# Kernel optimization log

Hardware: AMD Instinct MI355X
Metric: run time of the kernel (lower is better)

The kernel has to match this reference:

```python
import jax, jax.numpy as jnp
import numpy as np

B, S, E = 16, 1024, 1024  # flattened-softmax view requires S == E
EPS = 1e-5


def _ln(x, g, b):
    mu = jnp.mean(x, axis=-1, keepdims=True)
    var = jnp.var(x, axis=-1, keepdims=True)
    return (x - mu) * jax.lax.rsqrt(var + EPS) * g + b


def setup_inputs() -> dict:
    key = jax.random.key(0)
    ks = jax.random.split(key, 7)
    sc = 1.0 / np.sqrt(E)
    return {
        "pl_source": jax.random.normal(ks[0], (B, S, E), jnp.float32),
        "sam_source": jax.random.normal(ks[1], (B, S, E), jnp.float32),
        "Wq": jax.random.normal(ks[2], (E, E), jnp.float32) * sc,
        "Wk": jax.random.normal(ks[3], (E, E), jnp.float32) * sc,
        "Wv": jax.random.normal(ks[4], (E, E), jnp.float32) * sc,
        "ln1_g": jnp.ones((E,), jnp.float32),
        "ln1_b": jnp.zeros((E,), jnp.float32),
        "W1": jax.random.normal(ks[5], (E, 2 * E), jnp.float32) * sc,
        "W2": jax.random.normal(ks[6], (2 * E, E), jnp.float32) * (1.0 / np.sqrt(2 * E)),
        "ln2_g": jnp.ones((E,), jnp.float32),
        "ln2_b": jnp.zeros((E,), jnp.float32),
    }


def reference(pl_source, sam_source, Wq, Wk, Wv, ln1_g, ln1_b, W1, W2, ln2_g, ln2_b):
    q = jnp.einsum('bse,ef->bsf', pl_source, Wq)
    k = jnp.einsum('bse,ef->bsf', sam_source, Wk)
    v = jnp.einsum('bse,ef->bsf', sam_source, Wv)
    # scores [B,S,S], scaled by sqrt(head dim of q)
    scores = jnp.einsum('bsf,btf->bst', q, k) / jnp.sqrt(jnp.asarray(E, q.dtype))
    # non-standard: softmax over the WHOLE flattened score matrix per batch
    w = jax.nn.softmax(scores.reshape(B, S * S), axis=-1).reshape(B, S, E)  # S == E
    attn = jnp.einsum('bst,bte->bse', w, v)
    x = _ln(attn + pl_source, ln1_g, ln1_b)
    ff = jnp.einsum('bsh,he->bse', jnp.einsum('bse,eh->bsh', x, W1), W2)
    return _ln(ff + x, ln2_g, ln2_b)
```

## Files before the change

kernel.cpp:

```cpp
#include <hip/hip_runtime.h>
#include <hip/hip_bf16.h>
#include <type_traits>


typedef float  f32x4  __attribute__((ext_vector_type(4)));
typedef unsigned short u16x8 __attribute__((ext_vector_type(8)));
typedef unsigned short u16x4 __attribute__((ext_vector_type(4)));
typedef __bf16 bf16x8 __attribute__((ext_vector_type(8)));

__device__ __forceinline__ unsigned short f2bf(float f) {
  unsigned int u = __float_as_uint(f);
  u += 0x7fffu + ((u >> 16) & 1u);
  return (unsigned short)(u >> 16);
}
__device__ __forceinline__ float bf2f(unsigned short h) {
  return __uint_as_float(((unsigned int)h) << 16);
}

template<int SPLIT>
__device__ __forceinline__ void cvt8(const float4& a, const float4& b, u16x8& h, u16x8& l) {
  float f[8] = {a.x, a.y, a.z, a.w, b.x, b.y, b.z, b.w};
#pragma unroll
  for (int i = 0; i < 8; ++i) {
    unsigned short hb = f2bf(f[i]);
    h[i] = hb;
    if constexpr (SPLIT) l[i] = f2bf(f[i] - bf2f(hb));
  }
}

template<int AM, int BM, int CM>
__global__ __launch_bounds__(256, 2)
void gemm(const void* __restrict__ Av, const void* __restrict__ Bv,
          void* __restrict__ Cv, int M, int N, int K, int lda, int ldb,
          long sA, long sB, long sC, float scale, float beta)
{
  constexpr bool SA = (AM == 2), SB = (BM == 2);
  constexpr int NB = 2 + (SA ? 1 : 0) + (SB ? 1 : 0);
  constexpr int IAL = 2;
  constexpr int IBL = SA ? 3 : 2;
  __shared__ unsigned short sh[NB][4][128][8];

  const int t    = threadIdx.x;
  const int lane = t & 63;
  const int wave = t >> 6;
  const int wm   = (wave >> 1) << 6;
  const int wn   = (wave & 1) << 6;
  const int bm   = blockIdx.x << 7;
  const int bn   = blockIdx.y << 7;
  const int r_   = t >> 1;
  const int g_   = t & 1;

  const unsigned short* A16 = (const unsigned short*)Av + (size_t)blockIdx.z * sA + (size_t)(bm + r_) * lda + (g_ << 3);
  const float*          A32 = (const float*)Av          + (size_t)blockIdx.z * sA + (size_t)(bm + r_) * lda + (g_ << 3);
  const unsigned short* B16 = (const unsigned short*)Bv + (size_t)blockIdx.z * sB + (size_t)(bn + r_) * ldb + (g_ << 3);
  const float*          B32 = (const float*)Bv          + (size_t)blockIdx.z * sB + (size_t)(bn + r_) * ldb + (g_ << 3);

  f32x4 acc[4][4];
#pragma unroll
  for (int mi = 0; mi < 4; ++mi)
#pragma unroll
    for (int ni = 0; ni < 4; ++ni)
      acc[mi][ni] = (f32x4){0.f, 0.f, 0.f, 0.f};

  u16x8 ha0, ha1, hb0, hb1;
  float4 fa0, fa1, fa2, fa3, fb0, fb1, fb2, fb3;

  auto loadAB = [&](int kt) {
    const int ko = kt << 5;
    if constexpr (AM == 0) {
      ha0 = *(const u16x8*)(A16 + ko);
      ha1 = *(const u16x8*)(A16 + ko + 16);
    } else {
      fa0 = *(const float4*)(A32 + ko);      fa1 = *(const float4*)(A32 + ko + 4);
      fa2 = *(const float4*)(A32 + ko + 16); fa3 = *(const float4*)(A32 + ko + 20);
    }
    if constexpr (BM == 0) {
      hb0 = *(const u16x8*)(B16 + ko);
      hb1 = *(const u16x8*)(B16 + ko + 16);
    } else {
      fb0 = *(const float4*)(B32 + ko);      fb1 = *(const float4*)(B32 + ko + 4);
      fb2 = *(const float4*)(B32 + ko + 16); fb3 = *(const float4*)(B32 + ko + 20);
    }
  };
  loadAB(0);

  const int NT = K >> 5;
  const int kg = lane >> 4;
  const int lr = lane & 15;

  for (int kt = 0; kt < NT; ++kt) {
    __syncthreads();
    if constexpr (AM == 0) {
      *(u16x8*)&sh[0][g_][r_][0]     = ha0;
      *(u16x8*)&sh[0][g_ + 2][r_][0] = ha1;
    } else {
      u16x8 h, l;
      cvt8<SA>(fa0, fa1, h, l);
      *(u16x8*)&sh[0][g_][r_][0] = h;     if constexpr (SA) *(u16x8*)&sh[IAL][g_][r_][0] = l;
      cvt8<SA>(fa2, fa3, h, l);
      *(u16x8*)&sh[0][g_ + 2][r_][0] = h; if constexpr (SA) *(u16x8*)&sh[IAL][g_ + 2][r_][0] = l;
    }
    if constexpr (BM == 0) {
      *(u16x8*)&sh[1][g_][r_][0]     = hb0;
      *(u16x8*)&sh[1][g_ + 2][r_][0] = hb1;
    } else {
      u16x8 h, l;
      cvt8<SB>(fb0, fb1, h, l);
      *(u16x8*)&sh[1][g_][r_][0] = h;     if constexpr (SB) *(u16x8*)&sh[IBL][g_][r_][0] = l;
      cvt8<SB>(fb2, fb3, h, l);
      *(u16x8*)&sh[1][g_ + 2][r_][0] = h; if constexpr (SB) *(u16x8*)&sh[IBL][g_ + 2][r_][0] = l;
    }
    __syncthreads();

    if (kt + 1 < NT) loadAB(kt + 1);

    u16x8 va_[4], vb_[4], val_[4], vbl_[4];
#pragma unroll
    for (int mi = 0; mi < 4; ++mi) {
      va_[mi] = *(const u16x8*)&sh[0][kg][wm + (mi << 4) + lr][0];
      if constexpr (SA) val_[mi] = *(const u16x8*)&sh[IAL][kg][wm + (mi << 4) + lr][0];
    }
#pragma unroll
    for (int ni = 0; ni < 4; ++ni) {
      vb_[ni] = *(const u16x8*)&sh[1][kg][wn + (ni << 4) + lr][0];
      if constexpr (SB) vbl_[ni] = *(const u16x8*)&sh[IBL][kg][wn + (ni << 4) + lr][0];
    }
#pragma unroll
    for (int mi = 0; mi < 4; ++mi)
#pragma unroll
      for (int ni = 0; ni < 4; ++ni) {
        acc[mi][ni] = __builtin_amdgcn_mfma_f32_16x16x32_bf16(
            __builtin_bit_cast(bf16x8, va_[mi]), __builtin_bit_cast(bf16x8, vb_[ni]),
            acc[mi][ni], 0, 0, 0);
        if constexpr (SB)
          acc[mi][ni] = __builtin_amdgcn_mfma_f32_16x16x32_bf16(
              __builtin_bit_cast(bf16x8, va_[mi]), __builtin_bit_cast(bf16x8, vbl_[ni]),
              acc[mi][ni], 0, 0, 0);
        if constexpr (SA)
          acc[mi][ni] = __builtin_amdgcn_mfma_f32_16x16x32_bf16(
              __builtin_bit_cast(bf16x8, val_[mi]), __builtin_bit_cast(bf16x8, vb_[ni]),
              acc[mi][ni], 0, 0, 0);
      }
  }

  const size_t cbase = (size_t)blockIdx.z * sC;
#pragma unroll
  for (int mi = 0; mi < 4; ++mi)
#pragma unroll
    for (int ni = 0; ni < 4; ++ni) {
      const int row0 = bm + wm + (mi << 4) + ((lane >> 4) << 2);
      const int col  = bn + wn + (ni << 4) + lr;
#pragma unroll
      for (int i = 0; i < 4; ++i) {
        float val = acc[mi][ni][i] * scale;
        const size_t idx = cbase + (size_t)(row0 + i) * N + col;
        if constexpr (CM == 0) {
          float* C = (float*)Cv;
          if (beta != 0.f) val += beta * C[idx];
          C[idx] = val;
        } else {
          ((unsigned short*)Cv)[idx] = f2bf(val);
        }
      }
    }
}

template<typename IT, typename OT>
__global__ __launch_bounds__(256)
void transpose_k(const IT* __restrict__ in, OT* __restrict__ out,
                 int R, int C, long sIn, long sOut)
{
  __shared__ float tile[32][33];
  in  += (size_t)blockIdx.z * sIn;
  out += (size_t)blockIdx.z * sOut;
  const int tx = threadIdx.x, ty = threadIdx.y;
  const int c0 = blockIdx.x << 5, r0 = blockIdx.y << 5;
#pragma unroll
  for (int i = 0; i < 4; ++i) {
    int r = ty + (i << 3);
    float v;
    if constexpr (std::is_same_v<IT, unsigned short>)
      v = bf2f(in[(size_t)(r0 + r) * C + c0 + tx]);
    else
      v = in[(size_t)(r0 + r) * C + c0 + tx];
    tile[r][tx] = v;
  }
  __syncthreads();
#pragma unroll
  for (int i = 0; i < 4; ++i) {
    int r = ty + (i << 3);
    float v = tile[tx][r];
    if constexpr (std::is_same_v<OT, unsigned short>)
      out[(size_t)(c0 + r) * R + r0 + tx] = f2bf(v);
    else
      out[(size_t)(c0 + r) * R + r0 + tx] = v;
  }
}

__global__ __launch_bounds__(256)
void softmax_pass1(const float* __restrict__ sc, float2* __restrict__ part)
{
  const int b = blockIdx.y;
  const float* p = sc + ((size_t)b << 20) + ((size_t)blockIdx.x << 12);
  const int t = threadIdx.x;
  float v[16];
#pragma unroll
  for (int i = 0; i < 4; ++i) {
    float4 f = *(const float4*)(p + (t << 2) + (i << 10));
    v[i * 4 + 0] = f.x; v[i * 4 + 1] = f.y; v[i * 4 + 2] = f.z; v[i * 4 + 3] = f.w;
  }
  float m = v[0];
#pragma unroll
  for (int i = 1; i < 16; ++i) m = fmaxf(m, v[i]);
  for (int off = 32; off; off >>= 1) m = fmaxf(m, __shfl_down(m, off));
  __shared__ float red[8];
  if ((t & 63) == 0) red[t >> 6] = m;
  __syncthreads();
  m = fmaxf(fmaxf(red[0], red[1]), fmaxf(red[2], red[3]));
  float s = 0.f;
#pragma unroll
  for (int i = 0; i < 16; ++i) s += __expf(v[i] - m);
  for (int off = 32; off; off >>= 1) s += __shfl_down(s, off);
  if ((t & 63) == 0) red[4 + (t >> 6)] = s;
  __syncthreads();
  if (t == 0) part[(b << 8) + blockIdx.x] = make_float2(m, red[4] + red[5] + red[6] + red[7]);
}

__global__ __launch_bounds__(256)
void softmax_pass2(const float2* __restrict__ part, float2* __restrict__ bstats)
{
  const int b = blockIdx.x, t = threadIdx.x;
  float2 pr = part[(b << 8) + t];
  float m = pr.x;
  for (int off = 32; off; off >>= 1) m = fmaxf(m, __shfl_down(m, off));
  __shared__ float red[8];
  if ((t & 63) == 0) red[t >> 6] = m;
  __syncthreads();
  m = fmaxf(fmaxf(red[0], red[1]), fmaxf(red[2], red[3]));
  float s = pr.y * __expf(pr.x - m);
  for (int off = 32; off; off >>= 1) s += __shfl_down(s, off);
  __shared__ float red2[4];
  if ((t & 63) == 0) red2[t >> 6] = s;
  __syncthreads();
  if (t == 0) bstats[b] = make_float2(m, 1.f / (red2[0] + red2[1] + red2[2] + red2[3]));
}

__global__ __launch_bounds__(256)
void softmax_pass3(const float* __restrict__ sc, unsigned short* __restrict__ wb,
                   const float2* __restrict__ bst)
{
  const int b = blockIdx.y;
  const float2 st = bst[b];
  const size_t off = ((size_t)b << 20) + ((size_t)blockIdx.x << 12) + ((size_t)threadIdx.x << 2);
  const float* p = sc + off;
  unsigned short* o = wb + off;
#pragma unroll
  for (int i = 0; i < 4; ++i) {
    float4 f = *(const float4*)(p + (i << 10));
    u16x4 u;
    u[0] = f2bf(__expf(f.x - st.x) * st.y);
    u[1] = f2bf(__expf(f.y - st.x) * st.y);
    u[2] = f2bf(__expf(f.z - st.x) * st.y);
    u[3] = f2bf(__expf(f.w - st.x) * st.y);
    *(u16x4*)(o + (i << 10)) = u;
  }
}

template<typename TA>
__global__ __launch_bounds__(256)
void ln_fused(const TA* __restrict__ a, const float* __restrict__ res,
              const float* __restrict__ g, const float* __restrict__ bb,
              float* __restrict__ out)
{
  const size_t base = (size_t)blockIdx.x << 10;
  const int t = threadIdx.x;
  float x0, x1, x2, x3;
  if constexpr (std::is_same_v<TA, unsigned short>) {
    u16x4 va = *(const u16x4*)(a + base + (t << 2));
    x0 = bf2f(va[0]); x1 = bf2f(va[1]); x2 = bf2f(va[2]); x3 = bf2f(va[3]);
  } else {
    float4 va = *(const float4*)(a + base + (t << 2));
    x0 = va.x; x1 = va.y; x2 = va.z; x3 = va.w;
  }
  float4 vr = *(const float4*)(res + base + (t << 2));
  x0 += vr.x; x1 += vr.y; x2 += vr.z; x3 += vr.w;
  float s = x0 + x1 + x2 + x3;
  float q = x0 * x0 + x1 * x1 + x2 * x2 + x3 * x3;
  for (int off = 32; off; off >>= 1) { s += __shfl_down(s, off); q += __shfl_down(q, off); }
  __shared__ float red[8];
  if ((t & 63) == 0) { red[t >> 6] = s; red[4 + (t >> 6)] = q; }
  __syncthreads();
  float S = red[0] + red[1] + red[2] + red[3];
  float Q = red[4] + red[5] + red[6] + red[7];
  float mu   = S * 0.0009765625f;
  float rstd = rsqrtf(Q * 0.0009765625f - mu * mu + 1e-5f);
  float4 vg = *(const float4*)(g + (t << 2));
  float4 vb = *(const float4*)(bb + (t << 2));
  float4 o;
  o.x = (x0 - mu) * rstd * vg.x + vb.x;
  o.y = (x1 - mu) * rstd * vg.y + vb.y;
  o.z = (x2 - mu) * rstd * vg.z + vb.z;
  o.w = (x3 - mu) * rstd * vg.w + vb.w;
  *(float4*)(out + base + (t << 2)) = o;
}

extern "C" void kernel_launch(void* const* d_in, const int* in_sizes, int n_in,
                              void* d_out, int out_size, void* d_ws, size_t ws_size,
                              hipStream_t stream)
{
  const float* pl  = (const float*)d_in[0];
  const float* sam = (const float*)d_in[1];
  const float* Wq  = (const float*)d_in[2];
  const float* Wk  = (const float*)d_in[3];
  const float* Wv  = (const float*)d_in[4];
  const float* g1  = (const float*)d_in[5];
  const float* b1  = (const float*)d_in[6];
  const float* W1  = (const float*)d_in[7];
  const float* W2  = (const float*)d_in[8];
  const float* g2  = (const float*)d_in[9];
  const float* b2  = (const float*)d_in[10];

  char* wsb = (char*)d_ws;
  const size_t MB = 1ull << 20;
  unsigned short* WqTb = (unsigned short*)(wsb + 0 * MB);
  unsigned short* WkTb = (unsigned short*)(wsb + 2 * MB);
  unsigned short* WvTb = (unsigned short*)(wsb + 4 * MB);
  float*  W1T  = (float*)(wsb + 6 * MB);
  float*  W2T  = (float*)(wsb + 14 * MB);
  unsigned short* qb   = (unsigned short*)(wsb + 22 * MB);
  unsigned short* kb   = (unsigned short*)(wsb + 54 * MB);
  unsigned short* vb   = (unsigned short*)(wsb + 86 * MB);
  unsigned short* vTb  = (unsigned short*)(wsb + 118 * MB);
  float*  hbuf  = (float*)(wsb + 86 * MB);
  float*  ffbuf = (float*)(wsb + 22 * MB);
  float*  sc    = (float*)(wsb + 150 * MB);
  float*  xbuf  = sc;
  float2* part  = (float2*)(wsb + 214 * MB);
  float2* bst   = (float2*)(wsb + 214 * MB + 65536);
  unsigned short* attnb = qb;
  unsigned short* wb_   = kb;

  const long M1 = 1 << 20;
  dim3 tb(32, 8);

  transpose_k<float, unsigned short><<<dim3(32, 32, 1), tb, 0, stream>>>(Wq, WqTb, 1024, 1024, 0, 0);
  transpose_k<float, unsigned short><<<dim3(32, 32, 1), tb, 0, stream>>>(Wk, WkTb, 1024, 1024, 0, 0);
  transpose_k<float, unsigned short><<<dim3(32, 32, 1), tb, 0, stream>>>(Wv, WvTb, 1024, 1024, 0, 0);
  transpose_k<float, float><<<dim3(64, 32, 1), tb, 0, stream>>>(W1, W1T, 1024, 2048, 0, 0);
  transpose_k<float, float><<<dim3(32, 64, 1), tb, 0, stream>>>(W2, W2T, 2048, 1024, 0, 0);

  gemm<1, 0, 1><<<dim3(128, 8, 1), 256, 0, stream>>>(pl,  WqTb, qb, 16384, 1024, 1024, 1024, 1024, 0, 0, 0, 1.f, 0.f);
  gemm<1, 0, 1><<<dim3(128, 8, 1), 256, 0, stream>>>(sam, WkTb, kb, 16384, 1024, 1024, 1024, 1024, 0, 0, 0, 1.f, 0.f);
  gemm<1, 0, 1><<<dim3(128, 8, 1), 256, 0, stream>>>(sam, WvTb, vb, 16384, 1024, 1024, 1024, 1024, 0, 0, 0, 1.f, 0.f);

  transpose_k<unsigned short, unsigned short><<<dim3(32, 32, 16), tb, 0, stream>>>(vb, vTb, 1024, 1024, M1, M1);

  gemm<0, 0, 0><<<dim3(8, 8, 16), 256, 0, stream>>>(qb, kb, sc, 1024, 1024, 1024, 1024, 1024, M1, M1, M1, 0.03125f, 0.f);

  softmax_pass1<<<dim3(256, 16, 1), 256, 0, stream>>>(sc, part);
  softmax_pass2<<<16, 256, 0, stream>>>(part, bst);
  softmax_pass3<<<dim3(256, 16, 1), 256, 0, stream>>>(sc, wb_, bst);

  gemm<0, 0, 1><<<dim3(8, 8, 16), 256, 0, stream>>>(wb_, vTb, attnb, 1024, 1024, 1024, 1024, 1024, M1, M1, M1, 1.f, 0.f);

  ln_fused<unsigned short><<<16384, 256, 0, stream>>>(attnb, pl, g1, b1, xbuf);

  gemm<2, 2, 0><<<dim3(128, 8, 1), 256, 0, stream>>>(xbuf, W1T,              hbuf,  16384, 1024, 1024, 1024, 1024, 0, 0, 0, 1.f, 0.f);
  gemm<2, 2, 0><<<dim3(128, 8, 1), 256, 0, stream>>>(hbuf, W2T,              ffbuf, 16384, 1024, 1024, 1024, 2048, 0, 0, 0, 1.f, 0.f);
  gemm<2, 2, 0><<<dim3(128, 8, 1), 256, 0, stream>>>(xbuf, W1T + (1024*1024), hbuf,  16384, 1024, 1024, 1024, 1024, 0, 0, 0, 1.f, 0.f);
  gemm<2, 2, 0><<<dim3(128, 8, 1), 256, 0, stream>>>(hbuf, W2T + 1024,        ffbuf, 16384, 1024, 1024, 1024, 2048, 0, 0, 0, 1.f, 1.f);

  ln_fused<float><<<16384, 256, 0, stream>>>(ffbuf, xbuf, g2, b2, (float*)d_out);
}
```

Baseline: 1.137 ms.

## Rework GEMM pipeline around 16-bit inputs with fp16 hi/lo split for FFN

```diff
diff --git a/kernel.cpp b/kernel.cpp
--- a/kernel.cpp
+++ b/kernel.cpp
@@ -1,44 +1,39 @@
 #include <hip/hip_runtime.h>
-#include <hip/hip_bf16.h>
-#include <type_traits>
-
-
-typedef float  f32x4  __attribute__((ext_vector_type(4)));
+
+
+typedef float  f32x4 __attribute__((ext_vector_type(4)));
+typedef unsigned short u16;
 typedef unsigned short u16x8 __attribute__((ext_vector_type(8)));
 typedef unsigned short u16x4 __attribute__((ext_vector_type(4)));
 typedef __bf16 bf16x8 __attribute__((ext_vector_type(8)));
-
-__device__ __forceinline__ unsigned short f2bf(float f) {
+typedef _Float16 f16x8 __attribute__((ext_vector_type(8)));
+
+__device__ __forceinline__ u16 f2bf(float f) {
   unsigned int u = __float_as_uint(f);
   u += 0x7fffu + ((u >> 16) & 1u);
-  return (unsigned short)(u >> 16);
-}
-__device__ __forceinline__ float bf2f(unsigned short h) {
+  return (u16)(u >> 16);
+}
+__device__ __forceinline__ float bf2f(u16 h) {
   return __uint_as_float(((unsigned int)h) << 16);
 }
-
-template<int SPLIT>
-__device__ __forceinline__ void cvt8(const float4& a, const float4& b, u16x8& h, u16x8& l) {
-  float f[8] = {a.x, a.y, a.z, a.w, b.x, b.y, b.z, b.w};
-#pragma unroll
-  for (int i = 0; i < 8; ++i) {
-    unsigned short hb = f2bf(f[i]);
-    h[i] = hb;
-    if constexpr (SPLIT) l[i] = f2bf(f[i] - bf2f(hb));
-  }
-}
-
-template<int AM, int BM, int CM>
-__global__ __launch_bounds__(256, 2)
-void gemm(const void* __restrict__ Av, const void* __restrict__ Bv,
-          void* __restrict__ Cv, int M, int N, int K, int lda, int ldb,
-          long sA, long sB, long sC, float scale, float beta)
-{
-  constexpr bool SA = (AM == 2), SB = (BM == 2);
-  constexpr int NB = 2 + (SA ? 1 : 0) + (SB ? 1 : 0);
-  constexpr int IAL = 2;
-  constexpr int IBL = SA ? 3 : 2;
-  __shared__ unsigned short sh[NB][4][128][8];
+__device__ __forceinline__ u16 f2h(float f) {
+  _Float16 h = (_Float16)f;
+  return __builtin_bit_cast(unsigned short, h);
+}
+__device__ __forceinline__ float h2f(u16 b) {
+  return (float)__builtin_bit_cast(_Float16, b);
+}
+
+template<int DT, int CM>
+__global__ __launch_bounds__(256)
+void gemm16(const u16* __restrict__ A0, const u16* __restrict__ A1,
+            const u16* __restrict__ B0, const u16* __restrict__ B1,
+            void* __restrict__ C0, void* __restrict__ C1,
+            int M, int N, int nseg, int lda, int ldb,
+            long batchA, long batchB, long batchC, float scale, float beta)
+{
+  __shared__ u16 lA[4096];
+  __shared__ u16 lB[4096];
 
   const int t    = threadIdx.x;
   const int lane = t & 63;
@@ -47,13 +42,20 @@
   const int wn   = (wave & 1) << 6;
   const int bm   = blockIdx.x << 7;
   const int bn   = blockIdx.y << 7;
-  const int r_   = t >> 1;
-  const int g_   = t & 1;
-
-  const unsigned short* A16 = (const unsigned short*)Av + (size_t)blockIdx.z * sA + (size_t)(bm + r_) * lda + (g_ << 3);
-  const float*          A32 = (const float*)Av          + (size_t)blockIdx.z * sA + (size_t)(bm + r_) * lda + (g_ << 3);
-  const unsigned short* B16 = (const unsigned short*)Bv + (size_t)blockIdx.z * sB + (size_t)(bn + r_) * ldb + (g_ << 3);
-  const float*          B32 = (const float*)Bv          + (size_t)blockIdx.z * sB + (size_t)(bn + r_) * ldb + (g_ << 3);
+
+  A0 += (size_t)blockIdx.z * batchA;  A1 += (size_t)blockIdx.z * batchA;
+  B0 += (size_t)blockIdx.z * batchB;  B1 += (size_t)blockIdx.z * batchB;
+
+  const int sr  = t >> 2;
+  const int scc = (t & 3) << 3;
+  const size_t aoff0 = (size_t)(bm + sr) * lda + scc;
+  const size_t aoff1 = (size_t)(bm + 64 + sr) * lda + scc;
+  const size_t boff0 = (size_t)(bn + sr) * ldb + scc;
+  const size_t boff1 = (size_t)(bn + 64 + sr) * ldb + scc;
+  u16* sA0 = &lA[t << 3];
+  u16* sA1 = &lA[2048 + (t << 3)];
+  u16* sB0 = &lB[t << 3];
+  u16* sB1 = &lB[2048 + (t << 3)];
 
   f32x4 acc[4][4];
 #pragma unroll
@@ -62,88 +64,56 @@
     for (int ni = 0; ni < 4; ++ni)
       acc[mi][ni] = (f32x4){0.f, 0.f, 0.f, 0.f};
 
-  u16x8 ha0, ha1, hb0, hb1;
-  float4 fa0, fa1, fa2, fa3, fb0, fb1, fb2, fb3;
-
-  auto loadAB = [&](int kt) {
-    const int ko = kt << 5;
-    if constexpr (AM == 0) {
-      ha0 = *(const u16x8*)(A16 + ko);
-      ha1 = *(const u16x8*)(A16 + ko + 16);
-    } else {
-      fa0 = *(const float4*)(A32 + ko);      fa1 = *(const float4*)(A32 + ko + 4);
-      fa2 = *(const float4*)(A32 + ko + 16); fa3 = *(const float4*)(A32 + ko + 20);
-    }
-    if constexpr (BM == 0) {
-      hb0 = *(const u16x8*)(B16 + ko);
-      hb1 = *(const u16x8*)(B16 + ko + 16);
-    } else {
-      fb0 = *(const float4*)(B32 + ko);      fb1 = *(const float4*)(B32 + ko + 4);
-      fb2 = *(const float4*)(B32 + ko + 16); fb3 = *(const float4*)(B32 + ko + 20);
-    }
-  };
-  loadAB(0);
-
-  const int NT = K >> 5;
   const int kg = lane >> 4;
   const int lr = lane & 15;
+  const int NT = nseg << 5;
+
+  u16x8 ra0 = *(const u16x8*)(A0 + aoff0);
+  u16x8 ra1 = *(const u16x8*)(A0 + aoff1);
+  u16x8 rb0 = *(const u16x8*)(B0 + boff0);
+  u16x8 rb1 = *(const u16x8*)(B0 + boff1);
 
   for (int kt = 0; kt < NT; ++kt) {
     __syncthreads();
-    if constexpr (AM == 0) {
-      *(u16x8*)&sh[0][g_][r_][0]     = ha0;
-      *(u16x8*)&sh[0][g_ + 2][r_][0] = ha1;
-    } else {
-      u16x8 h, l;
-      cvt8<SA>(fa0, fa1, h, l);
-      *(u16x8*)&sh[0][g_][r_][0] = h;     if constexpr (SA) *(u16x8*)&sh[IAL][g_][r_][0] = l;
-      cvt8<SA>(fa2, fa3, h, l);
-      *(u16x8*)&sh[0][g_ + 2][r_][0] = h; if constexpr (SA) *(u16x8*)&sh[IAL][g_ + 2][r_][0] = l;
+    *(u16x8*)sA0 = ra0;
+    *(u16x8*)sA1 = ra1;
+    *(u16x8*)sB0 = rb0;
+    *(u16x8*)sB1 = rb1;
+    __syncthreads();
+
+    if (kt + 1 < NT) {
+      const u16* As = ((kt + 1) & 32) ? A1 : A0;
+      const u16* Bs = ((kt + 1) & 32) ? B1 : B0;
+      const int ko = ((kt + 1) & 31) << 5;
+      ra0 = *(const u16x8*)(As + aoff0 + ko);
+      ra1 = *(const u16x8*)(As + aoff1 + ko);
+      rb0 = *(const u16x8*)(Bs + boff0 + ko);
+      rb1 = *(const u16x8*)(Bs + boff1 + ko);
     }
-    if constexpr (BM == 0) {
-      *(u16x8*)&sh[1][g_][r_][0]     = hb0;
-      *(u16x8*)&sh[1][g_ + 2][r_][0] = hb1;
-    } else {
-      u16x8 h, l;
-      cvt8<SB>(fb0, fb1, h, l);
-      *(u16x8*)&sh[1][g_][r_][0] = h;     if constexpr (SB) *(u16x8*)&sh[IBL][g_][r_][0] = l;
-      cvt8<SB>(fb2, fb3, h, l);
-      *(u16x8*)&sh[1][g_ + 2][r_][0] = h; if constexpr (SB) *(u16x8*)&sh[IBL][g_ + 2][r_][0] = l;
-    }
-    __syncthreads();
-
-    if (kt + 1 < NT) loadAB(kt + 1);
-
-    u16x8 va_[4], vb_[4], val_[4], vbl_[4];
-#pragma unroll
-    for (int mi = 0; mi < 4; ++mi) {
-      va_[mi] = *(const u16x8*)&sh[0][kg][wm + (mi << 4) + lr][0];
-      if constexpr (SA) val_[mi] = *(const u16x8*)&sh[IAL][kg][wm + (mi << 4) + lr][0];
-    }
-#pragma unroll
-    for (int ni = 0; ni < 4; ++ni) {
-      vb_[ni] = *(const u16x8*)&sh[1][kg][wn + (ni << 4) + lr][0];
-      if constexpr (SB) vbl_[ni] = *(const u16x8*)&sh[IBL][kg][wn + (ni << 4) + lr][0];
-    }
+
+    u16x8 fa[4], fb[4];
 #pragma unroll
     for (int mi = 0; mi < 4; ++mi)
+      fa[mi] = *(const u16x8*)&lA[((wm + (mi << 4) + lr) << 5) + (kg << 3)];
+#pragma unroll
+    for (int ni = 0; ni < 4; ++ni)
+      fb[ni] = *(const u16x8*)&lB[((wn + (ni << 4) + lr) << 5) + (kg << 3)];
+#pragma unroll
+    for (int mi = 0; mi < 4; ++mi)
 #pragma unroll
       for (int ni = 0; ni < 4; ++ni) {
-        acc[mi][ni] = __builtin_amdgcn_mfma_f32_16x16x32_bf16(
-            __builtin_bit_cast(bf16x8, va_[mi]), __builtin_bit_cast(bf16x8, vb_[ni]),
-            acc[mi][ni], 0, 0, 0);
-        if constexpr (SB)
+        if constexpr (DT == 0)
           acc[mi][ni] = __builtin_amdgcn_mfma_f32_16x16x32_bf16(
-              __builtin_bit_cast(bf16x8, va_[mi]), __builtin_bit_cast(bf16x8, vbl_[ni]),
+              __builtin_bit_cast(bf16x8, fa[mi]), __builtin_bit_cast(bf16x8, fb[ni]),
               acc[mi][ni], 0, 0, 0);
-        if constexpr (SA)
-          acc[mi][ni] = __builtin_amdgcn_mfma_f32_16x16x32_bf16(
-              __builtin_bit_cast(bf16x8, val_[mi]), __builtin_bit_cast(bf16x8, vb_[ni]),
+        else
+          acc[mi][ni] = __builtin_amdgcn_mfma_f32_16x16x32_f16(
+              __builtin_bit_cast(f16x8, fa[mi]), __builtin_bit_cast(f16x8, fb[ni]),
               acc[mi][ni], 0, 0, 0);
       }
   }
 
-  const size_t cbase = (size_t)blockIdx.z * sC;
+  const size_t cb = (size_t)blockIdx.z * batchC;
 #pragma unroll
   for (int mi = 0; mi < 4; ++mi)
 #pragma unroll
@@ -152,37 +122,38 @@
       const int col  = bn + wn + (ni << 4) + lr;
 #pragma unroll
       for (int i = 0; i < 4; ++i) {
-        float val = acc[mi][ni][i] * scale;
-        const size_t idx = cbase + (size_t)(row0 + i) * N + col;
+        float v = acc[mi][ni][i] * scale;
+        const size_t idx = cb + (size_t)(row0 + i) * N + col;
         if constexpr (CM == 0) {
-          float* C = (float*)Cv;
-          if (beta != 0.f) val += beta * C[idx];
-          C[idx] = val;
+          float* C = (float*)C0;
+          if (beta != 0.f) v += beta * C[idx];
+          C[idx] = v;
+        } else if constexpr (CM == 1) {
+          ((u16*)C0)[idx] = f2bf(v);
         } else {
-          ((unsigned short*)Cv)[idx] = f2bf(val);
+          u16 hb = f2h(v);
+          ((u16*)C0)[idx] = hb;
+          ((u16*)C1)[idx] = f2h(v - h2f(hb));
         }
       }
     }
 }
 
-template<typename IT, typename OT>
-__global__ __launch_bounds__(256)
-void transpose_k(const IT* __restrict__ in, OT* __restrict__ out,
-                 int R, int C, long sIn, long sOut)
+template<int IM, int OM>
+__global__ __launch_bounds__(256)
+void transpose_cvt(const void* __restrict__ inv, u16* __restrict__ out,
+                   int R, int C, int ldin, int coff, long sIn, long sOut)
 {
   __shared__ float tile[32][33];
-  in  += (size_t)blockIdx.z * sIn;
-  out += (size_t)blockIdx.z * sOut;
   const int tx = threadIdx.x, ty = threadIdx.y;
   const int c0 = blockIdx.x << 5, r0 = blockIdx.y << 5;
 #pragma unroll
   for (int i = 0; i < 4; ++i) {
     int r = ty + (i << 3);
+    size_t idx = (size_t)blockIdx.z * sIn + (size_t)(r0 + r) * ldin + c0 + tx + coff;
     float v;
-    if constexpr (std::is_same_v<IT, unsigned short>)
-      v = bf2f(in[(size_t)(r0 + r) * C + c0 + tx]);
-    else
-      v = in[(size_t)(r0 + r) * C + c0 + tx];
+    if constexpr (IM == 0) v = ((const float*)inv)[idx];
+    else                   v = bf2f(((const u16*)inv)[idx]);
     tile[r][tx] = v;
   }
   __syncthreads();
@@ -190,10 +161,21 @@
   for (int i = 0; i < 4; ++i) {
     int r = ty + (i << 3);
     float v = tile[tx][r];
-    if constexpr (std::is_same_v<OT, unsigned short>)
-      out[(size_t)(c0 + r) * R + r0 + tx] = f2bf(v);
-    else
-      out[(size_t)(c0 + r) * R + r0 + tx] = v;
+    size_t idx = (size_t)blockIdx.z * sOut + (size_t)(c0 + r) * R + r0 + tx;
+    out[idx] = (OM == 1) ? f2bf(v) : f2h(v);
+  }
+}
+
+__global__ __launch_bounds__(256)
+void cvt_bf16k(const float* __restrict__ in, u16* __restrict__ out, int n4)
+{
+  int i = blockIdx.x * 256 + threadIdx.x;
+  const int stride = gridDim.x * 256;
+  for (; i < n4; i += stride) {
+    float4 f = ((const float4*)in)[i];
+    u16x4 o;
+    o[0] = f2bf(f.x); o[1] = f2bf(f.y); o[2] = f2bf(f.z); o[3] = f2bf(f.w);
+    ((u16x4*)out)[i] = o;
   }
 }
 
@@ -246,14 +228,14 @@
 }
 
 __global__ __launch_bounds__(256)
-void softmax_pass3(const float* __restrict__ sc, unsigned short* __restrict__ wb,
+void softmax_pass3(const float* __restrict__ sc, u16* __restrict__ wb,
                    const float2* __restrict__ bst)
 {
   const int b = blockIdx.y;
   const float2 st = bst[b];
   const size_t off = ((size_t)b << 20) + ((size_t)blockIdx.x << 12) + ((size_t)threadIdx.x << 2);
   const float* p = sc + off;
-  unsigned short* o = wb + off;
+  u16* o = wb + off;
 #pragma unroll
   for (int i = 0; i < 4; ++i) {
     float4 f = *(const float4*)(p + (i << 10));
@@ -266,26 +248,35 @@
   }
 }
 
-template<typename TA>
-__global__ __launch_bounds__(256)
-void ln_fused(const TA* __restrict__ a, const float* __restrict__ res,
-              const float* __restrict__ g, const float* __restrict__ bb,
-              float* __restrict__ out)
+template<int AM, int RM, int OM>
+__global__ __launch_bounds__(256)
+void ln_fused(const void* __restrict__ av, const void* __restrict__ r0v,
+              const void* __restrict__ r1v, const float* __restrict__ g,
+              const float* __restrict__ bb, void* __restrict__ o0v,
+              void* __restrict__ o1v)
 {
   const size_t base = (size_t)blockIdx.x << 10;
   const int t = threadIdx.x;
-  float x0, x1, x2, x3;
-  if constexpr (std::is_same_v<TA, unsigned short>) {
-    u16x4 va = *(const u16x4*)(a + base + (t << 2));
-    x0 = bf2f(va[0]); x1 = bf2f(va[1]); x2 = bf2f(va[2]); x3 = bf2f(va[3]);
+  float x[4];
+  if constexpr (AM == 0) {
+    float4 a = *(const float4*)((const float*)av + base + (t << 2));
+    x[0] = a.x; x[1] = a.y; x[2] = a.z; x[3] = a.w;
   } else {
-    float4 va = *(const float4*)(a + base + (t << 2));
-    x0 = va.x; x1 = va.y; x2 = va.z; x3 = va.w;
-  }
-  float4 vr = *(const float4*)(res + base + (t << 2));
-  x0 += vr.x; x1 += vr.y; x2 += vr.z; x3 += vr.w;
-  float s = x0 + x1 + x2 + x3;
-  float q = x0 * x0 + x1 * x1 + x2 * x2 + x3 * x3;
+    u16x4 a = *(const u16x4*)((const u16*)av + base + (t << 2));
+#pragma unroll
+    for (int i = 0; i < 4; ++i) x[i] = bf2f(a[i]);
+  }
+  if constexpr (RM == 0) {
+    float4 r = *(const float4*)((const float*)r0v + base + (t << 2));
+    x[0] += r.x; x[1] += r.y; x[2] += r.z; x[3] += r.w;
+  } else {
+    u16x4 rh = *(const u16x4*)((const u16*)r0v + base + (t << 2));
+    u16x4 rl = *(const u16x4*)((const u16*)r1v + base + (t << 2));
+#pragma unroll
+    for (int i = 0; i < 4; ++i) x[i] += h2f(rh[i]) + h2f(rl[i]);
+  }
+  float s = x[0] + x[1] + x[2] + x[3];
+  float q = x[0]*x[0] + x[1]*x[1] + x[2]*x[2] + x[3]*x[3];
   for (int off = 32; off; off >>= 1) { s += __shfl_down(s, off); q += __shfl_down(q, off); }
   __shared__ float red[8];
   if ((t & 63) == 0) { red[t >> 6] = s; red[4 + (t >> 6)] = q; }
@@ -296,12 +287,24 @@
   float rstd = rsqrtf(Q * 0.0009765625f - mu * mu + 1e-5f);
   float4 vg = *(const float4*)(g + (t << 2));
   float4 vb = *(const float4*)(bb + (t << 2));
-  float4 o;
-  o.x = (x0 - mu) * rstd * vg.x + vb.x;
-  o.y = (x1 - mu) * rstd * vg.y + vb.y;
-  o.z = (x2 - mu) * rstd * vg.z + vb.z;
-  o.w = (x3 - mu) * rstd * vg.w + vb.w;
-  *(float4*)(out + base + (t << 2)) = o;
+  float y[4];
+  y[0] = (x[0] - mu) * rstd * vg.x + vb.x;
+  y[1] = (x[1] - mu) * rstd * vg.y + vb.y;
+  y[2] = (x[2] - mu) * rstd * vg.z + vb.z;
+  y[3] = (x[3] - mu) * rstd * vg.w + vb.w;
+  if constexpr (OM == 0) {
+    float4 o = {y[0], y[1], y[2], y[3]};
+    *(float4*)((float*)o0v + base + (t << 2)) = o;
+  } else {
+    u16x4 oh, ol;
+#pragma unroll
+    for (int i = 0; i < 4; ++i) {
+      oh[i] = f2h(y[i]);
+      ol[i] = f2h(y[i] - h2f(oh[i]));
+    }
+    *(u16x4*)((u16*)o0v + base + (t << 2)) = oh;
+    *(u16x4*)((u16*)o1v + base + (t << 2)) = ol;
+  }
 }
 
 extern "C" void kernel_launch(void* const* d_in, const int* in_sizes, int n_in,
@@ -322,53 +325,64 @@
 
   char* wsb = (char*)d_ws;
   const size_t MB = 1ull << 20;
-  unsigned short* WqTb = (unsigned short*)(wsb + 0 * MB);
-  unsigned short* WkTb = (unsigned short*)(wsb + 2 * MB);
-  unsigned short* WvTb = (unsigned short*)(wsb + 4 * MB);
-  float*  W1T  = (float*)(wsb + 6 * MB);
-  float*  W2T  = (float*)(wsb + 14 * MB);
-  unsigned short* qb   = (unsigned short*)(wsb + 22 * MB);
-  unsigned short* kb   = (unsigned short*)(wsb + 54 * MB);
-  unsigned short* vb   = (unsigned short*)(wsb + 86 * MB);
-  unsigned short* vTb  = (unsigned short*)(wsb + 118 * MB);
-  float*  hbuf  = (float*)(wsb + 86 * MB);
-  float*  ffbuf = (float*)(wsb + 22 * MB);
-  float*  sc    = (float*)(wsb + 150 * MB);
-  float*  xbuf  = sc;
-  float2* part  = (float2*)(wsb + 214 * MB);
-  float2* bst   = (float2*)(wsb + 214 * MB + 65536);
-  unsigned short* attnb = qb;
-  unsigned short* wb_   = kb;
-
-  const long M1 = 1 << 20;
+  u16*   plb   = (u16*)(wsb + 0 * MB);
+  u16*   samb  = (u16*)(wsb + 32 * MB);
+  u16*   qb    = (u16*)(wsb + 64 * MB);
+  u16*   vTb   = (u16*)(wsb + 96 * MB);
+  u16*   kvb   = (u16*)(wsb + 128 * MB);
+  float* sc    = (float*)(wsb + 0 * MB);
+  u16*   wb    = qb;
+  u16*   attnb = kvb;
+  u16*   xh    = qb;
+  u16*   xl    = vTb;
+  u16*   hhH   = (u16*)(wsb + 0 * MB);
+  u16*   hlH   = (u16*)(wsb + 32 * MB);
+  float* ff    = (float*)(wsb + 128 * MB);
+  u16*   WqTb  = (u16*)(wsb + 192 * MB);
+  u16*   WkvTb = (u16*)(wsb + 194 * MB);
+  u16*   W1Th  = (u16*)(wsb + 198 * MB);
+  u16*   W2Th  = (u16*)(wsb + 202 * MB);
+  float2* part = (float2*)(wsb + 206 * MB);
+  float2* bst  = (float2*)(wsb + 206 * MB + 65536);
+
+  const long M1 = 1 << 20, M2 = 2 << 20;
   dim3 tb(32, 8);
 
-  transpose_k<float, unsigned short><<<dim3(32, 32, 1), tb, 0, stream>>>(Wq, WqTb, 1024, 1024, 0, 0);
-  transpose_k<float, unsigned short><<<dim3(32, 32, 1), tb, 0, stream>>>(Wk, WkTb, 1024, 1024, 0, 0);
-  transpose_k<float, unsigned short><<<dim3(32, 32, 1), tb, 0, stream>>>(Wv, WvTb, 1024, 1024, 0, 0);
-  transpose_k<float, float><<<dim3(64, 32, 1), tb, 0, stream>>>(W1, W1T, 1024, 2048, 0, 0);
-  transpose_k<float, float><<<dim3(32, 64, 1), tb, 0, stream>>>(W2, W2T, 2048, 1024, 0, 0);
-
-  gemm<1, 0, 1><<<dim3(128, 8, 1), 256, 0, stream>>>(pl,  WqTb, qb, 16384, 1024, 1024, 1024, 1024, 0, 0, 0, 1.f, 0.f);
-  gemm<1, 0, 1><<<dim3(128, 8, 1), 256, 0, stream>>>(sam, WkTb, kb, 16384, 1024, 1024, 1024, 1024, 0, 0, 0, 1.f, 0.f);
-  gemm<1, 0, 1><<<dim3(128, 8, 1), 256, 0, stream>>>(sam, WvTb, vb, 16384, 1024, 1024, 1024, 1024, 0, 0, 0, 1.f, 0.f);
-
-  transpose_k<unsigned short, unsigned short><<<dim3(32, 32, 16), tb, 0, stream>>>(vb, vTb, 1024, 1024, M1, M1);
-
-  gemm<0, 0, 0><<<dim3(8, 8, 16), 256, 0, stream>>>(qb, kb, sc, 1024, 1024, 1024, 1024, 1024, M1, M1, M1, 0.03125f, 0.f);
+  cvt_bf16k<<<2048, 256, 0, stream>>>(pl,  plb,  1 << 22);
+  cvt_bf16k<<<2048, 256, 0, stream>>>(sam, samb, 1 << 22);
+  transpose_cvt<0,1><<<dim3(32, 32, 1), tb, 0, stream>>>(Wq, WqTb, 1024, 1024, 1024, 0, 0, 0);
+  transpose_cvt<0,1><<<dim3(32, 32, 1), tb, 0, stream>>>(Wk, WkvTb, 1024, 1024, 1024, 0, 0, 0);
+  transpose_cvt<0,1><<<dim3(32, 32, 1), tb, 0, stream>>>(Wv, WkvTb + M1, 1024, 1024, 1024, 0, 0, 0);
+  transpose_cvt<0,2><<<dim3(64, 32, 1), tb, 0, stream>>>(W1, W1Th, 1024, 2048, 2048, 0, 0, 0);
+  transpose_cvt<0,2><<<dim3(32, 64, 1), tb, 0, stream>>>(W2, W2Th, 2048, 1024, 1024, 0, 0, 0);
+
+  gemm16<0,1><<<dim3(128, 8, 1), 256, 0, stream>>>(plb, plb, WqTb, WqTb, qb, nullptr,
+      16384, 1024, 1, 1024, 1024, 0, 0, 0, 1.f, 0.f);
+  gemm16<0,1><<<dim3(128, 16, 1), 256, 0, stream>>>(samb, samb, WkvTb, WkvTb, kvb, nullptr,
+      16384, 2048, 1, 1024, 1024, 0, 0, 0, 1.f, 0.f);
+
+  transpose_cvt<1,1><<<dim3(32, 32, 16), tb, 0, stream>>>(kvb, vTb, 1024, 1024, 2048, 1024, M2, M1);
+
+  gemm16<0,0><<<dim3(8, 8, 16), 256, 0, stream>>>(qb, qb, kvb, kvb, sc, nullptr,
+      1024, 1024, 1, 1024, 2048, M1, M2, M1, 0.03125f, 0.f);
 
   softmax_pass1<<<dim3(256, 16, 1), 256, 0, stream>>>(sc, part);
   softmax_pass2<<<16, 256, 0, stream>>>(part, bst);
-  softmax_pass3<<<dim3(256, 16, 1), 256, 0, stream>>>(sc, wb_, bst);
-
-  gemm<0, 0, 1><<<dim3(8, 8, 16), 256, 0, stream>>>(wb_, vTb, attnb, 1024, 1024, 1024, 1024, 1024, M1, M1, M1, 1.f, 0.f);
-
-  ln_fused<unsigned short><<<16384, 256, 0, stream>>>(attnb, pl, g1, b1, xbuf);
-
-  gemm<2, 2, 0><<<dim3(128, 8, 1), 256, 0, stream>>>(xbuf, W1T,              hbuf,  16384, 1024, 1024, 1024, 1024, 0, 0, 0, 1.f, 0.f);
-  gemm<2, 2, 0><<<dim3(128, 8, 1), 256, 0, stream>>>(hbuf, W2T,              ffbuf, 16384, 1024, 1024, 1024, 2048, 0, 0, 0, 1.f, 0.f);
-  gemm<2, 2, 0><<<dim3(128, 8, 1), 256, 0, stream>>>(xbuf, W1T + (1024*1024), hbuf,  16384, 1024, 1024, 1024, 1024, 0, 0, 0, 1.f, 0.f);
-  gemm<2, 2, 0><<<dim3(128, 8, 1), 256, 0, stream>>>(hbuf, W2T + 1024,        ffbuf, 16384, 1024, 1024, 1024, 2048, 0, 0, 0, 1.f, 1.f);
-
-  ln_fused<float><<<16384, 256, 0, stream>>>(ffbuf, xbuf, g2, b2, (float*)d_out);
-}
+  softmax_pass3<<<dim3(256, 16, 1), 256, 0, stream>>>(sc, wb, bst);
+
+  gemm16<0,1><<<dim3(8, 8, 16), 256, 0, stream>>>(wb, wb, vTb, vTb, attnb, nullptr,
+      1024, 1024, 1, 1024, 1024, M1, M1, M1, 1.f, 0.f);
+
+  ln_fused<1,0,1><<<16384, 256, 0, stream>>>(attnb, pl, nullptr, g1, b1, xh, xl);
+
+  gemm16<1,2><<<dim3(128, 8, 1), 256, 0, stream>>>(xh, xl, W1Th, W1Th, hhH, hlH,
+      16384, 1024, 2, 1024, 1024, 0, 0, 0, 1.f, 0.f);
+  gemm16<1,0><<<dim3(128, 8, 1), 256, 0, stream>>>(hhH, hlH, W2Th, W2Th, ff, nullptr,
+      16384, 1024, 2, 1024, 2048, 0, 0, 0, 1.f, 0.f);
+  gemm16<1,2><<<dim3(128, 8, 1), 256, 0, stream>>>(xh, xl, W1Th + M1, W1Th + M1, hhH, hlH,
+      16384, 1024, 2, 1024, 1024, 0, 0, 0, 1.f, 0.f);
+  gemm16<1,0><<<dim3(128, 8, 1), 256, 0, stream>>>(hhH, hlH, W2Th + 1024, W2Th + 1024, ff, nullptr,
+      16384, 1024, 2, 1024, 2048, 0, 0, 0, 1.f, 1.f);
+
+  ln_fused<0,1,0><<<16384, 256, 0, stream>>>(ff, xh, xl, g2, b2, d_out, nullptr);
+}
```

Measured after the change: 1.024 ms. -10.0%, faster.
